# Kernel optimization log

Hardware: AMD Instinct MI355X
Metric: run time of the kernel (lower is better)

## Reference

```python
import jax, jax.numpy as jnp
import numpy as np

TOP_K = 2  # routing_method: renormalize top-2 (topk then softmax over selected logits)


def setup_inputs() -> dict:
    key = jax.random.key(0)
    ks = jax.random.split(key, 5)
    T, H, I, E = 4096, 1024, 4096, 8
    return {
        "hidden_states": jax.random.normal(ks[0], (T, H), jnp.float32),
        "router_logits": jax.random.normal(ks[1], (T, E), jnp.float32),
        "W_gate": jax.random.normal(ks[2], (E, H, I), jnp.float32) * 0.02,  # w1
        "W_up": jax.random.normal(ks[3], (E, H, I), jnp.float32) * 0.02,   # w3
        "W_down": jax.random.normal(ks[4], (E, I, H), jnp.float32) * 0.02, # w2
    }


def reference(hidden_states, router_logits, W_gate, W_up, W_down):
    # Routing: top-k logits, renormalize with softmax over selected logits.
    top_vals, top_idx = jax.lax.top_k(router_logits, TOP_K)        # [T, K]
    routing_weights = jax.nn.softmax(top_vals, axis=-1)            # [T, K]

    E = W_gate.shape[0]
    out = jnp.zeros_like(hidden_states)                            # [T, H]
    for e in range(E):  # fixed small expert loop (structurally distinct weights)
        # combine weight for expert e per token (0 if not routed here)
        w_e = jnp.sum(jnp.where(top_idx == e, routing_weights, 0.0), axis=-1)  # [T]
        gate = hidden_states @ W_gate[e]                           # [T, I]
        up = hidden_states @ W_up[e]                               # [T, I]
        y = (jax.nn.silu(gate) * up) @ W_down[e]                   # [T, H]
        out = out + w_e[:, None] * y
    return out
```

## Files before the change

kernel.cpp:

```cpp
#include <hip/hip_runtime.h>

typedef float    f32x4  __attribute__((ext_vector_type(4)));
typedef float    f32x16 __attribute__((ext_vector_type(16)));
typedef _Float16 f16x8  __attribute__((ext_vector_type(8)));
typedef _Float16 f16x4  __attribute__((ext_vector_type(4)));

#define T_TOK 4096
#define HD    1024
#define ID    4096
#define NE    8
#define TOTP  (2*T_TOK)
#define MAXT1 72
#define MAXT2 40

#define WS_CNT   0
#define WS_FILL  64
#define WS_OFF   128
#define WS_TOT   192
#define WS_TOT2  196
#define WS_TEXP  256
#define WS_TM0   (256 + 4*MAXT1)
#define WS_TEXP2 (256 + 8*MAXT1)
#define WS_TM02  (256 + 8*MAXT1 + 4*MAXT2)
#define WS_TOPE  2048
#define WS_TOPW  (WS_TOPE + 4*TOTP)
#define WS_PAIR  (WS_TOPW + 4*TOTP)
#define WS_ACT   ((size_t)1 << 20)
constexpr size_t WS_YBUF = WS_ACT  + 2ull*TOTP*ID;
constexpr size_t WS_HS16 = WS_YBUF + 2ull*TOTP*HD;
constexpr size_t WS_WG16 = WS_HS16 + 2ull*T_TOK*HD;
constexpr size_t WS_WU16 = WS_WG16 + 2ull*NE*HD*ID;
constexpr size_t WS_WD16 = WS_WU16 + 2ull*NE*HD*ID;
constexpr size_t WS_YB   = WS_WG16;

__device__ __forceinline__ void gll16(const void* g, void* l) {
  __builtin_amdgcn_global_load_lds(
      (const __attribute__((address_space(1))) unsigned int*)g,
      (__attribute__((address_space(3))) unsigned int*)l, 16, 0, 0);
}

#define WAITV(N) do { \
    asm volatile("s_waitcnt vmcnt(" #N ")" ::: "memory"); \
    __builtin_amdgcn_sched_barrier(0); \
  } while (0)

__device__ __forceinline__ int lofs64(int row, int g8) {
  return row * 64 + ((g8 ^ (row & 7)) << 3);
}

__global__ void k_router(const float* __restrict__ logits, char* __restrict__ ws) {
  int t = blockIdx.x * blockDim.x + threadIdx.x;
  if (t >= T_TOK) return;
  float v0 = -1e30f, v1 = -1e30f; int i0 = 0, i1 = 0;
  #pragma unroll
  for (int e = 0; e < NE; ++e) {
    float v = logits[t * NE + e];
    if (v > v0)      { v1 = v0; i1 = i0; v0 = v; i0 = e; }
    else if (v > v1) { v1 = v;  i1 = e; }
  }
  float w0 = 1.f / (1.f + __expf(v1 - v0));
  ((int*)(ws + WS_TOPE))[2*t]   = i0;
  ((int*)(ws + WS_TOPE))[2*t+1] = i1;
  ((float*)(ws + WS_TOPW))[2*t]   = w0;
  ((float*)(ws + WS_TOPW))[2*t+1] = 1.f - w0;
  atomicAdd(&((int*)(ws + WS_CNT))[i0], 1);
  atomicAdd(&((int*)(ws + WS_CNT))[i1], 1);
}

__global__ void k_prefix(char* __restrict__ ws) {
  if (threadIdx.x != 0 || blockIdx.x != 0) return;
  const int* cnt = (const int*)(ws + WS_CNT);
  int* off   = (int*)(ws + WS_OFF);
  int* texp  = (int*)(ws + WS_TEXP);
  int* tm0   = (int*)(ws + WS_TM0);
  int* texp2 = (int*)(ws + WS_TEXP2);
  int* tm02  = (int*)(ws + WS_TM02);
  int run = 0, t1 = 0, t2 = 0;
  for (int e = 0; e < NE; ++e) {
    off[e] = run;
    int ne = cnt[e];
    for (int i = 0; i < ne; i += 128) { texp[t1] = e; tm0[t1] = i; ++t1; }
    for (int i = 0; i < ne; i += 256) { texp2[t2] = e; tm02[t2] = i; ++t2; }
    run += ne;
  }
  off[NE] = run;
  *(int*)(ws + WS_TOT)  = t1;
  *(int*)(ws + WS_TOT2) = t2;
}

__global__ void k_scatter(char* __restrict__ ws) {
  int t = blockIdx.x * blockDim.x + threadIdx.x;
  if (t >= T_TOK) return;
  const int* tope = (const int*)(ws + WS_TOPE);
  const int* off  = (const int*)(ws + WS_OFF);
  int* fill = (int*)(ws + WS_FILL);
  int* pair = (int*)(ws + WS_PAIR);
  #pragma unroll
  for (int s = 0; s < 2; ++s) {
    int id = 2*t + s;
    int e = tope[id];
    int pos = off[e] + atomicAdd(&fill[e], 1);
    pair[pos] = id;
  }
}

__global__ void k_hscvt(const float* __restrict__ src, _Float16* __restrict__ dst) {
  int i = blockIdx.x * blockDim.x + threadIdx.x;
  f32x4 v = ((const f32x4*)src)[i];
  f16x4 o;
  #pragma unroll
  for (int j = 0; j < 4; ++j) o[j] = (_Float16)v[j];
  ((f16x4*)dst)[i] = o;
}

__global__ __launch_bounds__(256) void k_wtrans(const float* __restrict__ src,
                                                _Float16* __restrict__ dst,
                                                int K, int N) {
  const int e = blockIdx.z;
  const int n0 = blockIdx.x * 64, k0 = blockIdx.y * 64;
  const float* s = src + (size_t)e * K * N;
  _Float16* d = dst + (size_t)e * (size_t)K * N;
  __shared__ _Float16 t[64][68];
  const int tx = threadIdx.x & 15, ty = threadIdx.x >> 4;
  #pragma unroll
  for (int it = 0; it < 4; ++it) {
    int k = k0 + it*16 + ty;
    f32x4 v = *(const f32x4*)&s[(size_t)k * N + n0 + tx*4];
    #pragma unroll
    for (int j = 0; j < 4; ++j) t[tx*4 + j][it*16 + ty] = (_Float16)v[j];
  }
  __syncthreads();
  #pragma unroll
  for (int it = 0; it < 4; ++it) {
    int n = it*16 + ty;
    *(f16x4*)&d[(size_t)(n0 + n) * K + k0 + tx*4] = *(const f16x4*)&t[n][tx*4];
  }
}

__global__ __launch_bounds__(512, 2) void k_gemm1(
    const _Float16* __restrict__ hs16, const _Float16* __restrict__ WgT,
    const _Float16* __restrict__ WuT, char* __restrict__ ws) {
  const int s = blockIdx.y;
  if (s >= *(const int*)(ws + WS_TOT2)) return;
  const int e    = ((const int*)(ws + WS_TEXP2))[s];
  const int m0   = ((const int*)(ws + WS_TM02))[s];
  const int offE = ((const int*)(ws + WS_OFF))[e];
  const int nE   = ((const int*)(ws + WS_CNT))[e];
  _Float16* __restrict__ act = (_Float16*)(ws + WS_ACT);
  const int n0 = blockIdx.x * 128;
  const int tid = threadIdx.x, lane = tid & 63, wid = tid >> 6;

  __shared__ __align__(16) _Float16 sm[2 * 32768];

  const int r8 = lane >> 3;
  const int q64 = (((lane & 7) ^ r8) << 3);
  const int* __restrict__ pairp = (const int*)(ws + WS_PAIR);
  const _Float16 *aP[4], *gP[2], *uP[2];
  #pragma unroll
  for (int c = 0; c < 4; ++c) {
    int mm = m0 + 32*wid + 8*c + r8;
    int tok = (mm < nE) ? (pairp[offE + mm] >> 1) : 0;
    aP[c] = hs16 + (size_t)tok * HD + q64;
  }
  #pragma unroll
  for (int c = 0; c < 2; ++c) {
    size_t col = (size_t)e * ID + (n0 + 16*wid + 8*c + r8);
    gP[c] = WgT + col * HD + q64;
    uP[c] = WuT + col * HD + q64;
  }

  auto stage8 = [&](int buf, int kt) {
    _Float16* base = sm + buf * 32768;
    const int ko = kt * 64;
    #pragma unroll
    for (int c = 0; c < 4; ++c)
      gll16(aP[c] + ko, base + (32*wid + 8*c) * 64);
    #pragma unroll
    for (int c = 0; c < 2; ++c) {
      gll16(gP[c] + ko, base + 16384 + (16*wid + 8*c) * 64);
      gll16(uP[c] + ko, base + 24576 + (16*wid + 8*c) * 64);
    }
  };

  const int wr = wid >> 2, wc = wid & 3;
  const int l31 = lane & 31, kh = lane >> 5;
  f32x16 accg[4] = {}, accu[4] = {};

  auto computeKK = [&](int buf, int kk) {
    const _Float16* b0 = sm + buf * 32768;
    f16x8 afr[4], bgf, buf_;
    #pragma unroll
    for (int i = 0; i < 4; ++i)
      afr[i] = *(const f16x8*)&b0[lofs64(128*wr + 32*i + l31, kk*2 + kh)];
    bgf  = *(const f16x8*)&b0[16384 + lofs64(32*wc + l31, kk*2 + kh)];
    buf_ = *(const f16x8*)&b0[24576 + lofs64(32*wc + l31, kk*2 + kh)];
    __builtin_amdgcn_s_setprio(1);
    #pragma unroll
    for (int i = 0; i < 4; ++i) {
      accg[i] = __builtin_amdgcn_mfma_f32_32x32x16_f16(afr[i], bgf,  accg[i], 0, 0, 0);
      accu[i] = __builtin_amdgcn_mfma_f32_32x32x16_f16(afr[i], buf_, accu[i], 0, 0, 0);
    }
    __builtin_amdgcn_s_setprio(0);
  };

  const int KT = HD / 64;
  stage8(0, 0);
  WAITV(0);
  __builtin_amdgcn_s_barrier();
  for (int t = 0; t < KT; ++t) {
    const int cur = t & 1;
    if (t + 1 < KT) stage8(cur ^ 1, t + 1);
    computeKK(cur, 0); computeKK(cur, 1);
    computeKK(cur, 2); computeKK(cur, 3);
    WAITV(0);
    __builtin_amdgcn_s_barrier();
  }

  #pragma unroll
  for (int i = 0; i < 4; ++i)
    #pragma unroll
    for (int r = 0; r < 16; ++r) {
      const int row = (r & 3) + 8 * (r >> 2) + 4 * kh;
      const int mm = m0 + 128*wr + 32*i + row;
      if (mm < nE) {
        float g = accg[i][r], u = accu[i][r];
        float sv = g / (1.f + __expf(-g)) * u;
        act[(size_t)(offE + mm) * ID + n0 + 32*wc + l31] = (_Float16)sv;
      }
    }
}

__global__ __launch_bounds__(512, 2) void k_gemm2(const _Float16* __restrict__ WdT,
                                                  char* __restrict__ ws) {
  const int s = blockIdx.y;
  if (s >= *(const int*)(ws + WS_TOT2)) return;
  const int e    = ((const int*)(ws + WS_TEXP2))[s];
  const int m0   = ((const int*)(ws + WS_TM02))[s];
  const int offE = ((const int*)(ws + WS_OFF))[e];
  const int nE   = ((const int*)(ws + WS_CNT))[e];
  const int h    = blockIdx.z;
  const int kbase = h * (ID / 2);
  const int* __restrict__ pair = (const int*)(ws + WS_PAIR);
  const _Float16* __restrict__ act = (const _Float16*)(ws + WS_ACT);
  _Float16* __restrict__ yb = (_Float16*)(ws + WS_YB) + (size_t)h * TOTP * HD;
  const int n0 = blockIdx.x * 256;
  const int tid = threadIdx.x, lane = tid & 63, wid = tid >> 6;

  __shared__ __align__(16) _Float16 sm[2 * 32768];

  const int r8 = lane >> 3;
  const int q64 = (((lane & 7) ^ r8) << 3);
  const _Float16 *aP[4], *bP[4];
  #pragma unroll
  for (int c = 0; c < 4; ++c) {
    int mm = m0 + 32*wid + 8*c + r8;
    int p = (mm < nE) ? (offE + mm) : offE;
    aP[c] = act + (size_t)p * ID + kbase + q64;
  }
  #pragma unroll
  for (int c = 0; c < 4; ++c)
    bP[c] = WdT + ((size_t)e * HD + (n0 + 32*wid + 8*c + r8)) * ID + kbase + q64;

  auto stage8 = [&](int buf, int kt) {
    _Float16* base = sm + buf * 32768;
    const int ko = kt * 64;
    #pragma unroll
    for (int c = 0; c < 4; ++c)
      gll16(aP[c] + ko, base + (32*wid + 8*c) * 64);
    #pragma unroll
    for (int c = 0; c < 4; ++c)
      gll16(bP[c] + ko, base + 16384 + (32*wid + 8*c) * 64);
  };

  const int wr = wid >> 2, wc = wid & 3;
  const int l31 = lane & 31, kh = lane >> 5;
  f32x16 acc[4][2] = {};

  auto computeKK = [&](int buf, int kk) {
    const _Float16* b0 = sm + buf * 32768;
    f16x8 afr[4], bfr[2];
    #pragma unroll
    for (int i = 0; i < 4; ++i)
      afr[i] = *(const f16x8*)&b0[lofs64(128*wr + 32*i + l31, kk*2 + kh)];
    #pragma unroll
    for (int j = 0; j < 2; ++j)
      bfr[j] = *(const f16x8*)&b0[16384 + lofs64(64*wc + 32*j + l31, kk*2 + kh)];
    __builtin_amdgcn_s_setprio(1);
    #pragma unroll
    for (int i = 0; i < 4; ++i)
      #pragma unroll
      for (int j = 0; j < 2; ++j)
        acc[i][j] = __builtin_amdgcn_mfma_f32_32x32x16_f16(afr[i], bfr[j], acc[i][j], 0, 0, 0);
    __builtin_amdgcn_s_setprio(0);
  };

  const int KT = (ID / 2) / 64;
  stage8(0, 0);
  WAITV(0);
  __builtin_amdgcn_s_barrier();
  for (int t = 0; t < KT; ++t) {
    const int cur = t & 1;
    if (t + 1 < KT) stage8(cur ^ 1, t + 1);
    computeKK(cur, 0); computeKK(cur, 1);
    computeKK(cur, 2); computeKK(cur, 3);
    WAITV(0);
    __builtin_amdgcn_s_barrier();
  }

  #pragma unroll
  for (int i = 0; i < 4; ++i)
    #pragma unroll
    for (int r = 0; r < 16; ++r) {
      const int row = (r & 3) + 8 * (r >> 2) + 4 * kh;
      const int mm = m0 + 128*wr + 32*i + row;
      if (mm < nE) {
        const int id = pair[offE + mm];
        #pragma unroll
        for (int j = 0; j < 2; ++j)
          yb[(size_t)id * HD + n0 + 64*wc + 32*j + l31] = (_Float16)acc[i][j][r];
      }
    }
}

__global__ void k_combine(const char* __restrict__ ws, float* __restrict__ out) {
  const int idx = blockIdx.x * blockDim.x + threadIdx.x;
  const int t = idx >> 7, c = idx & 127;
  const float* topw = (const float*)(ws + WS_TOPW);
  const _Float16* yb = (const _Float16*)(ws + WS_YB);
  float s0[8] = {}, s1[8] = {};
  #pragma unroll
  for (int h = 0; h < 2; ++h) {
    const _Float16* p = yb + (size_t)h * TOTP * HD;
    f16x8 y0 = ((const f16x8*)(p + (size_t)(2*t)     * HD))[c];
    f16x8 y1 = ((const f16x8*)(p + (size_t)(2*t + 1) * HD))[c];
    #pragma unroll
    for (int j = 0; j < 8; ++j) { s0[j] += (float)y0[j]; s1[j] += (float)y1[j]; }
  }
  const float w0 = topw[2*t], w1 = topw[2*t+1];
  f32x4 o0, o1;
  #pragma unroll
  for (int j = 0; j < 4; ++j) {
    o0[j] = w0 * s0[j]     + w1 * s1[j];
    o1[j] = w0 * s0[4 + j] + w1 * s1[4 + j];
  }
  ((f32x4*)out)[2*idx]     = o0;
  ((f32x4*)out)[2*idx + 1] = o1;
}

extern "C" void kernel_launch(void* const* d_in, const int* in_sizes, int n_in,
                              void* d_out, int out_size, void* d_ws, size_t ws_size,
                              hipStream_t stream) {
  const float* hs     = (const float*)d_in[0];
  const float* logits = (const float*)d_in[1];
  const float* Wg     = (const float*)d_in[2];
  const float* Wu     = (const float*)d_in[3];
  const float* Wd     = (const float*)d_in[4];
  char* ws = (char*)d_ws;

  _Float16* hs16 = (_Float16*)(ws + WS_HS16);
  _Float16* wg16 = (_Float16*)(ws + WS_WG16);
  _Float16* wu16 = (_Float16*)(ws + WS_WU16);
  _Float16* wd16 = (_Float16*)(ws + WS_WD16);

  hipMemsetAsync(ws, 0, 256, stream);
  k_router <<<dim3(T_TOK/256), dim3(256), 0, stream>>>(logits, ws);
  k_prefix <<<dim3(1),         dim3(64),  0, stream>>>(ws);
  k_scatter<<<dim3(T_TOK/256), dim3(256), 0, stream>>>(ws);
  k_hscvt  <<<dim3(T_TOK*HD/4/256), dim3(256), 0, stream>>>(hs, hs16);
  k_wtrans <<<dim3(ID/64, HD/64, NE), dim3(256), 0, stream>>>(Wg, wg16, HD, ID);
  k_wtrans <<<dim3(ID/64, HD/64, NE), dim3(256), 0, stream>>>(Wu, wu16, HD, ID);
  k_wtrans <<<dim3(HD/64, ID/64, NE), dim3(256), 0, stream>>>(Wd, wd16, ID, HD);
  k_gemm1  <<<dim3(ID/128, MAXT2),    dim3(512), 0, stream>>>(hs16, wg16, wu16, ws);
  k_gemm2  <<<dim3(HD/256, MAXT2, 2), dim3(512), 0, stream>>>(wd16, ws);
  k_combine<<<dim3(T_TOK*HD/8/256), dim3(256), 0, stream>>>(ws, (float*)d_out);
}
```

Before: 534.0 us.

## Switch GEMM LDS tiles to k-group-major layout, dropping XOR swizzle

Both expert GEMM kernels now stage tiles into LDS as [k-group][row][8] instead of row-major with an XOR swizzle. Each wave loads one 8-element k-slice for 64 consecutive rows, so the 16-byte LDS fragment reads by consecutive lanes become contiguous and conflict-free without swizzle arithmetic. The cost is that global loads within a wave now hit 64 different rows with 16 bytes each, which reduces coalescing per row and may increase memory transactions.

```diff
diff --git a/kernel.cpp b/kernel.cpp
--- a/kernel.cpp
+++ b/kernel.cpp
@@ -44,10 +44,6 @@
     __builtin_amdgcn_sched_barrier(0); \
   } while (0)
 
-__device__ __forceinline__ int lofs64(int row, int g8) {
-  return row * 64 + ((g8 ^ (row & 7)) << 3);
-}
-
 __global__ void k_router(const float* __restrict__ logits, char* __restrict__ ws) {
   int t = blockIdx.x * blockDim.x + threadIdx.x;
   if (t >= T_TOK) return;
@@ -152,21 +148,19 @@
 
   __shared__ __align__(16) _Float16 sm[2 * 32768];
 
-  const int r8 = lane >> 3;
-  const int q64 = (((lane & 7) ^ r8) << 3);
   const int* __restrict__ pairp = (const int*)(ws + WS_PAIR);
   const _Float16 *aP[4], *gP[2], *uP[2];
   #pragma unroll
   for (int c = 0; c < 4; ++c) {
-    int mm = m0 + 32*wid + 8*c + r8;
+    int mm = m0 + 64*c + lane;
     int tok = (mm < nE) ? (pairp[offE + mm] >> 1) : 0;
-    aP[c] = hs16 + (size_t)tok * HD + q64;
+    aP[c] = hs16 + (size_t)tok * HD + wid * 8;
   }
   #pragma unroll
   for (int c = 0; c < 2; ++c) {
-    size_t col = (size_t)e * ID + (n0 + 16*wid + 8*c + r8);
-    gP[c] = WgT + col * HD + q64;
-    uP[c] = WuT + col * HD + q64;
+    size_t col = (size_t)e * ID + (n0 + 64*c + lane);
+    gP[c] = WgT + col * HD + wid * 8;
+    uP[c] = WuT + col * HD + wid * 8;
   }
 
   auto stage8 = [&](int buf, int kt) {
@@ -174,11 +168,11 @@
     const int ko = kt * 64;
     #pragma unroll
     for (int c = 0; c < 4; ++c)
-      gll16(aP[c] + ko, base + (32*wid + 8*c) * 64);
+      gll16(aP[c] + ko, base + wid*2048 + c*512);
     #pragma unroll
     for (int c = 0; c < 2; ++c) {
-      gll16(gP[c] + ko, base + 16384 + (16*wid + 8*c) * 64);
-      gll16(uP[c] + ko, base + 24576 + (16*wid + 8*c) * 64);
+      gll16(gP[c] + ko, base + 16384 + wid*1024 + c*512);
+      gll16(uP[c] + ko, base + 24576 + wid*1024 + c*512);
     }
   };
 
@@ -188,12 +182,13 @@
 
   auto computeKK = [&](int buf, int kk) {
     const _Float16* b0 = sm + buf * 32768;
+    const int g = kk*2 + kh;
     f16x8 afr[4], bgf, buf_;
     #pragma unroll
     for (int i = 0; i < 4; ++i)
-      afr[i] = *(const f16x8*)&b0[lofs64(128*wr + 32*i + l31, kk*2 + kh)];
-    bgf  = *(const f16x8*)&b0[16384 + lofs64(32*wc + l31, kk*2 + kh)];
-    buf_ = *(const f16x8*)&b0[24576 + lofs64(32*wc + l31, kk*2 + kh)];
+      afr[i] = *(const f16x8*)&b0[g*2048 + (128*wr + 32*i + l31) * 8];
+    bgf  = *(const f16x8*)&b0[16384 + g*1024 + (32*wc + l31) * 8];
+    buf_ = *(const f16x8*)&b0[24576 + g*1024 + (32*wc + l31) * 8];
     __builtin_amdgcn_s_setprio(1);
     #pragma unroll
     for (int i = 0; i < 4; ++i) {
@@ -248,28 +243,26 @@
 
   __shared__ __align__(16) _Float16 sm[2 * 32768];
 
-  const int r8 = lane >> 3;
-  const int q64 = (((lane & 7) ^ r8) << 3);
   const _Float16 *aP[4], *bP[4];
   #pragma unroll
   for (int c = 0; c < 4; ++c) {
-    int mm = m0 + 32*wid + 8*c + r8;
+    int mm = m0 + 64*c + lane;
     int p = (mm < nE) ? (offE + mm) : offE;
-    aP[c] = act + (size_t)p * ID + kbase + q64;
+    aP[c] = act + (size_t)p * ID + kbase + wid * 8;
   }
   #pragma unroll
   for (int c = 0; c < 4; ++c)
-    bP[c] = WdT + ((size_t)e * HD + (n0 + 32*wid + 8*c + r8)) * ID + kbase + q64;
+    bP[c] = WdT + ((size_t)e * HD + (n0 + 64*c + lane)) * ID + kbase + wid * 8;
 
   auto stage8 = [&](int buf, int kt) {
     _Float16* base = sm + buf * 32768;
     const int ko = kt * 64;
     #pragma unroll
     for (int c = 0; c < 4; ++c)
-      gll16(aP[c] + ko, base + (32*wid + 8*c) * 64);
+      gll16(aP[c] + ko, base + wid*2048 + c*512);
     #pragma unroll
     for (int c = 0; c < 4; ++c)
-      gll16(bP[c] + ko, base + 16384 + (32*wid + 8*c) * 64);
+      gll16(bP[c] + ko, base + 16384 + wid*2048 + c*512);
   };
 
   const int wr = wid >> 2, wc = wid & 3;
@@ -278,13 +271,14 @@
 
   auto computeKK = [&](int buf, int kk) {
     const _Float16* b0 = sm + buf * 32768;
+    const int g = kk*2 + kh;
     f16x8 afr[4], bfr[2];
     #pragma unroll
     for (int i = 0; i < 4; ++i)
-      afr[i] = *(const f16x8*)&b0[lofs64(128*wr + 32*i + l31, kk*2 + kh)];
+      afr[i] = *(const f16x8*)&b0[g*2048 + (128*wr + 32*i + l31) * 8];
     #pragma unroll
     for (int j = 0; j < 2; ++j)
-      bfr[j] = *(const f16x8*)&b0[16384 + lofs64(64*wc + 32*j + l31, kk*2 + kh)];
+      bfr[j] = *(const f16x8*)&b0[16384 + g*2048 + (64*wc + 32*j + l31) * 8];
     __builtin_amdgcn_s_setprio(1);
     #pragma unroll
     for (int i = 0; i < 4; ++i)
```

Measured after the change: 615.1 us. 15.2% more time.
